# Kernel optimization log

Measured on AMD Instinct MI355X. Metric: run time of the kernel, lower is better.

The kernel has to match this reference:

```python
import jax, jax.numpy as jnp
import numpy as np

B = 16384      # batch
H = 1024       # latent_dim
C = 2          # output_dim (classes)
PPC = 24       # prototypes per class
P = C * PPC    # 48 total prototypes
EPS = 1e-4


def setup_inputs() -> dict:
    key = jax.random.key(0)
    k1, k2, k3, k4, k5 = jax.random.split(key, 5)
    specific_user = jax.random.normal(k1, (B, H), jnp.float32)
    shared_user = jax.random.normal(k2, (B, H), jnp.float32)
    prototype_vectors = jax.random.normal(k3, (P, H), jnp.float32)
    # last_layer weight set by set_last_layer_incorrect_connection(-0.5):
    # +1 for the prototype's own class, -0.5 elsewhere; shape [C, P]
    cls = np.arange(P) // PPC
    ident = (cls[None, :] == np.arange(C)[:, None]).astype(np.float32)
    last_layer_w = jnp.asarray(ident * 1.0 + (1.0 - ident) * (-0.5))
    # nn.Bilinear(H, H, 1): weight [1, H, H], bias [1]
    bilinear_w = jax.random.normal(k4, (1, H, H), jnp.float32) / np.sqrt(H)
    bilinear_b = jax.random.normal(k5, (1,), jnp.float32) * 0.01
    return {
        "specific_user": specific_user,
        "shared_user": shared_user,
        "prototype_vectors": prototype_vectors,
        "last_layer_w": last_layer_w,
        "bilinear_w": bilinear_w,
        "bilinear_b": bilinear_b,
        "flag": 1,
    }


def reference(specific_user, shared_user, prototype_vectors, last_layer_w,
              bilinear_w, bilinear_b, flag):
    # prototype_distances: squared euclid via mm + norms, then log-similarity
    x2 = jnp.sum(specific_user ** 2, axis=1, keepdims=True)          # [B,1]
    p2 = jnp.sum(prototype_vectors ** 2, axis=1)                     # [P]
    distance = -2.0 * (specific_user @ prototype_vectors.T) + x2 + p2[None, :]  # [B,P]
    similarity = jnp.log((distance + 1.0) / (distance + EPS))        # [B,P]
    logits = similarity @ last_layer_w.T                             # [B,C]

    # select the class's 24 prototypes (flag picks class 1 or 0; static int)
    idx = 1 if flag else 0
    sub = prototype_vectors.reshape(C, PPC, H)[idx]                  # [PPC,H]

    # prototype_subgraph_distances: per original broadcast, each row of
    # all_sim is the batch-mean of the log-similarity -> constant over batch.
    s2 = jnp.sum(sub ** 2, axis=1)                                   # [PPC]
    d = -2.0 * (specific_user @ sub.T) + x2 + s2[None, :]            # [B,PPC]
    sim = jnp.mean(jnp.log((d + 1.0) / (d + EPS)), axis=0)           # [PPC]
    jstar = jnp.argmax(sim)                                          # scalar
    chosen_proto = jnp.broadcast_to(sub[jstar], specific_user.shape) # [B,H]

    # nn.Bilinear(chosen_proto, shared_user) -> [B,1]
    pos = jnp.einsum('bi,ij,bj->b', chosen_proto, bilinear_w[0], shared_user)[:, None] + bilinear_b
    return (pos, shared_user, logits, distance)
```

## Files before the change

### kernel.cpp

```cpp
#include <hip/hip_runtime.h>
#include <hip/hip_bf16.h>

#define BATCH 16384
#define HD    1024
#define NP    48
#define PPC   24
#define EPSV  1e-4f

typedef __attribute__((ext_vector_type(8))) short  short8;
typedef __attribute__((ext_vector_type(4))) float  floatx4;

__device__ __forceinline__ float b2f(unsigned short s) {
    union { unsigned u; float f; } c; c.u = ((unsigned)s) << 16; return c.f;
}
__device__ __forceinline__ unsigned short f2bu(float f) {
    __hip_bfloat16 h = __float2bfloat16(f);
    union { __hip_bfloat16 h; unsigned short u; } c; c.h = h; return c.u;
}

__global__ __launch_bounds__(256) void k_prep(const float* __restrict__ proto,
                                              const float* __restrict__ w2,
                                              const int*   __restrict__ flag,
                                              unsigned short* __restrict__ phi,
                                              unsigned short* __restrict__ plo,
                                              float* __restrict__ p2,
                                              float* __restrict__ gcol,
                                              float* __restrict__ V) {
    const int bid = blockIdx.x;
    const int tid = threadIdx.x;

    if (bid < 48) {
        const int p = bid;
        if (p == 4 && tid < NP) gcol[tid] = 0.f;
        const float* row = proto + (size_t)p * HD;
        float acc = 0.f;
#pragma unroll
        for (int c = 0; c < 4; ++c) {
            const int k = c * 256 + tid;
            const float f = row[k];
            acc += f * f;
            const unsigned short h = f2bu(f);
            phi[(size_t)p * HD + k] = h;
            plo[(size_t)p * HD + k] = f2bu(f - b2f(h));
        }
#pragma unroll
        for (int m = 32; m >= 1; m >>= 1) acc += __shfl_xor(acc, m, 64);
        __shared__ float wsum[4];
        if ((tid & 63) == 0) wsum[tid >> 6] = acc;
        __syncthreads();
        if (tid == 0) p2[p] = wsum[0] + wsum[1] + wsum[2] + wsum[3];
    } else {
        const int q   = bid - 48;
        const int jg  = q >> 4;
        const int cc  = q & 15;
        const int c   = cc * 64 + (tid & 63);
        const int j   = jg * 4 + (tid >> 6);
        const int idx = (flag[0] != 0) ? 1 : 0;
        const float* prow = proto + (size_t)(idx * PPC + j) * HD;
        float acc = 0.f;
#pragma unroll 2
        for (int i = 0; i < HD; i += 4) {
            const floatx4 pv = *(const floatx4*)(prow + i);
            acc += pv[0] * w2[(size_t)(i + 0) * HD + c];
            acc += pv[1] * w2[(size_t)(i + 1) * HD + c];
            acc += pv[2] * w2[(size_t)(i + 2) * HD + c];
            acc += pv[3] * w2[(size_t)(i + 3) * HD + c];
        }
        V[(size_t)j * HD + c] = acc;
    }
}

__global__ __launch_bounds__(256, 4) void k_main(
    const float* __restrict__ x,
    const unsigned short* __restrict__ phi,
    const unsigned short* __restrict__ plo,
    const float* __restrict__ llw,
    const float* __restrict__ p2,
    float* __restrict__ gcol,
    float* __restrict__ out_logits,
    float* __restrict__ out_dist)
{
    __shared__ float lacc[4][64][13];
    __shared__ float lx2[4][16];
    const int wave = threadIdx.x >> 6;
    const int lane = threadIdx.x & 63;
    const int quad = lane >> 4;
    const int lr   = lane & 15;
    const int rb   = blockIdx.x * 16;
    const int ko   = wave * 256;

    const float* xr = x + (size_t)(rb + lr) * HD + ko + quad * 8;
    const unsigned short* ph0 = phi + (size_t)lr * HD + ko + quad * 8;
    const unsigned short* ph1 = ph0 + 16 * HD;
    const unsigned short* ph2 = ph0 + 32 * HD;
    const unsigned short* pl0 = plo + (size_t)lr * HD + ko + quad * 8;
    const unsigned short* pl1 = pl0 + 16 * HD;
    const unsigned short* pl2 = pl0 + 32 * HD;

    floatx4 acc0 = {0.f, 0.f, 0.f, 0.f};
    floatx4 acc1 = {0.f, 0.f, 0.f, 0.f};
    floatx4 acc2 = {0.f, 0.f, 0.f, 0.f};
    float x2p = 0.f;

#pragma unroll 2
    for (int kk = 0; kk < 8; ++kk) {
        const floatx4 xa = *(const floatx4*)(xr + kk * 32);
        const floatx4 xb = *(const floatx4*)(xr + kk * 32 + 4);
        short8 ah, al;
#pragma unroll
        for (int j = 0; j < 4; ++j) {
            const float f = xa[j];
            x2p += f * f;
            const unsigned short h = f2bu(f);
            ah[j] = (short)h;
            al[j] = (short)f2bu(f - b2f(h));
        }
#pragma unroll
        for (int j = 0; j < 4; ++j) {
            const float f = xb[j];
            x2p += f * f;
            const unsigned short h = f2bu(f);
            ah[4 + j] = (short)h;
            al[4 + j] = (short)f2bu(f - b2f(h));
        }
        const short8 bh0 = *(const short8*)(ph0 + kk * 32);
        const short8 bh1 = *(const short8*)(ph1 + kk * 32);
        const short8 bh2 = *(const short8*)(ph2 + kk * 32);
        const short8 bl0 = *(const short8*)(pl0 + kk * 32);
        const short8 bl1 = *(const short8*)(pl1 + kk * 32);
        const short8 bl2 = *(const short8*)(pl2 + kk * 32);
        acc0 = __builtin_amdgcn_mfma_f32_16x16x32_bf16(ah, bh0, acc0, 0, 0, 0);
        acc0 = __builtin_amdgcn_mfma_f32_16x16x32_bf16(ah, bl0, acc0, 0, 0, 0);
        acc0 = __builtin_amdgcn_mfma_f32_16x16x32_bf16(al, bh0, acc0, 0, 0, 0);
        acc1 = __builtin_amdgcn_mfma_f32_16x16x32_bf16(ah, bh1, acc1, 0, 0, 0);
        acc1 = __builtin_amdgcn_mfma_f32_16x16x32_bf16(ah, bl1, acc1, 0, 0, 0);
        acc1 = __builtin_amdgcn_mfma_f32_16x16x32_bf16(al, bh1, acc1, 0, 0, 0);
        acc2 = __builtin_amdgcn_mfma_f32_16x16x32_bf16(ah, bh2, acc2, 0, 0, 0);
        acc2 = __builtin_amdgcn_mfma_f32_16x16x32_bf16(ah, bl2, acc2, 0, 0, 0);
        acc2 = __builtin_amdgcn_mfma_f32_16x16x32_bf16(al, bh2, acc2, 0, 0, 0);
    }
    x2p += __shfl_xor(x2p, 16, 64);
    x2p += __shfl_xor(x2p, 32, 64);

#pragma unroll
    for (int r = 0; r < 4; ++r) {
        lacc[wave][lane][r]     = acc0[r];
        lacc[wave][lane][4 + r] = acc1[r];
        lacc[wave][lane][8 + r] = acc2[r];
    }
    if (quad == 0) lx2[wave][lr] = x2p;
    __syncthreads();
    if (wave != 0) return;

    float facc[12];
#pragma unroll
    for (int i = 0; i < 12; ++i)
        facc[i] = lacc[0][lane][i] + lacc[1][lane][i] + lacc[2][lane][i] + lacc[3][lane][i];
    const float x2full = lx2[0][lr] + lx2[1][lr] + lx2[2][lr] + lx2[3][lr];

    float s0[4] = {0.f, 0.f, 0.f, 0.f};
    float s1[4] = {0.f, 0.f, 0.f, 0.f};

#pragma unroll
    for (int t = 0; t < 3; ++t) {
        const int p = t * 16 + lr;
        const float p2p = p2[p];
        const float w0 = llw[p];
        const float w1 = llw[NP + p];
        float cst = 0.f;
#pragma unroll
        for (int r = 0; r < 4; ++r) {
            const int row = quad * 4 + r;
            const float x2r = __shfl(x2full, row, 64);
            const float d = -2.f * facc[t * 4 + r] + x2r + p2p;
            out_dist[(size_t)(rb + row) * NP + p] = d;
            const float sim = log1pf((1.f - EPSV) / (d + EPSV));
            s0[r] += sim * w0;
            s1[r] += sim * w1;
            cst += sim;
        }
        cst += __shfl_xor(cst, 16, 64);
        cst += __shfl_xor(cst, 32, 64);
        if (quad == 0) atomicAdd(&gcol[p], cst);
    }

#pragma unroll
    for (int r = 0; r < 4; ++r) {
        float r0 = s0[r], r1 = s1[r];
#pragma unroll
        for (int m = 1; m <= 8; m <<= 1) {
            r0 += __shfl_xor(r0, m, 64);
            r1 += __shfl_xor(r1, m, 64);
        }
        if (lr == 0) {
            const int brow = rb + quad * 4 + r;
            out_logits[(size_t)brow * 2 + 0] = r0;
            out_logits[(size_t)brow * 2 + 1] = r1;
        }
    }
}

__global__ __launch_bounds__(256) void k_pos(
    const float* __restrict__ sh,
    const float* __restrict__ V,
    const float* __restrict__ gcol,
    const int*   __restrict__ flag,
    const float* __restrict__ bias,
    float* __restrict__ out_pos,
    float* __restrict__ out_copy)
{
    __shared__ int js;
    const int tid  = threadIdx.x;
    if (tid == 0) {
        const int idx = (flag[0] != 0) ? 1 : 0;
        const float* cs = gcol + idx * PPC;
        int bj = 0; float bv = cs[0];
        for (int j = 1; j < PPC; ++j)
            if (cs[j] > bv) { bv = cs[j]; bj = j; }
        js = bj;
    }
    __syncthreads();

    const int wave = tid >> 6;
    const int lane = tid & 63;
    const int b = blockIdx.x * 4 + wave;

    const floatx4* src = (const floatx4*)(sh + (size_t)b * HD);
    floatx4* dst = (floatx4*)(out_copy + (size_t)b * HD);
    const floatx4* vv = (const floatx4*)(V + (size_t)js * HD);
    float acc = 0.f;
#pragma unroll
    for (int c = 0; c < 4; ++c) {
        const int idx2 = c * 64 + lane;
        const floatx4 r = src[idx2];
        __builtin_nontemporal_store(r, &dst[idx2]);
        const floatx4 vr = vv[idx2];
#pragma unroll
        for (int j = 0; j < 4; ++j) acc += r[j] * vr[j];
    }
#pragma unroll
    for (int m = 1; m <= 32; m <<= 1) acc += __shfl_xor(acc, m, 64);
    if (lane == 0) out_pos[b] = acc + bias[0];
}

extern "C" void kernel_launch(void* const* d_in, const int* in_sizes, int n_in,
                              void* d_out, int out_size, void* d_ws, size_t ws_size,
                              hipStream_t stream) {
    const float* x     = (const float*)d_in[0];
    const float* sh    = (const float*)d_in[1];
    const float* proto = (const float*)d_in[2];
    const float* llw   = (const float*)d_in[3];
    const float* w2    = (const float*)d_in[4];
    const float* bb    = (const float*)d_in[5];
    const int*   flag  = (const int*)d_in[6];

    float* out = (float*)d_out;
    float* out_pos    = out;
    float* out_copy   = out + BATCH;
    float* out_logits = out + BATCH + BATCH * HD;
    float* out_dist   = out + BATCH + BATCH * HD + BATCH * 2;

    float* ws_col = (float*)d_ws;
    float* ws_p2  = ws_col + 64;
    float* ws_V   = ws_col + 1024;
    unsigned short* ws_phi = (unsigned short*)(ws_col + 25600);
    unsigned short* ws_plo = ws_phi + NP * HD;

    k_prep<<<144, 256, 0, stream>>>(proto, w2, flag, ws_phi, ws_plo, ws_p2, ws_col, ws_V);
    k_main<<<1024, 256, 0, stream>>>(x, ws_phi, ws_plo, llw, ws_p2, ws_col, out_logits, out_dist);
    k_pos<<<4096, 256, 0, stream>>>(sh, ws_V, ws_col, flag, bb, out_pos, out_copy);
}
```

Measured before the change: 282.6 us.

## Split V=P·W2 over K chunks with register-blocked partials, reduce in main kernel

The prototype-by-bilinear-weight product in the prep kernel is restructured. Before, each thread computed one output column for one prototype over the full 1024-long reduction, rereading W2 once per prototype group. Now each block takes a 64-row slice of W2 and caches the 24 prototype slices in shared memory. Each thread keeps 24 accumulators, so every W2 element is loaded once, and the block writes partial sums to a workspace. Extra blocks appended to the main kernel add up the 16 partials. This costs more workspace traffic and register pressure, and it relies on launch order within the stream so that the reduction runs before k_pos reads V.

```diff
diff --git a/kernel.cpp b/kernel.cpp
--- a/kernel.cpp
+++ b/kernel.cpp
@@ -25,7 +25,7 @@
                                               unsigned short* __restrict__ plo,
                                               float* __restrict__ p2,
                                               float* __restrict__ gcol,
-                                              float* __restrict__ V) {
+                                              float* __restrict__ Vp) {
     const int bid = blockIdx.x;
     const int tid = threadIdx.x;
 
@@ -50,23 +50,32 @@
         __syncthreads();
         if (tid == 0) p2[p] = wsum[0] + wsum[1] + wsum[2] + wsum[3];
     } else {
-        const int q   = bid - 48;
-        const int jg  = q >> 4;
-        const int cc  = q & 15;
-        const int c   = cc * 64 + (tid & 63);
-        const int j   = jg * 4 + (tid >> 6);
+        __shared__ float pl[24][64];
+        const int q  = bid - 48;
+        const int ic = q >> 2;
+        const int cc = q & 3;
+        const int i0 = ic * 64;
+        const int c  = cc * 256 + tid;
         const int idx = (flag[0] != 0) ? 1 : 0;
-        const float* prow = proto + (size_t)(idx * PPC + j) * HD;
-        float acc = 0.f;
-#pragma unroll 2
-        for (int i = 0; i < HD; i += 4) {
-            const floatx4 pv = *(const floatx4*)(prow + i);
-            acc += pv[0] * w2[(size_t)(i + 0) * HD + c];
-            acc += pv[1] * w2[(size_t)(i + 1) * HD + c];
-            acc += pv[2] * w2[(size_t)(i + 2) * HD + c];
-            acc += pv[3] * w2[(size_t)(i + 3) * HD + c];
-        }
-        V[(size_t)j * HD + c] = acc;
+
+        for (int t = tid; t < 24 * 64; t += 256) {
+            const int j = t >> 6, i = t & 63;
+            pl[j][i] = proto[(size_t)(idx * PPC + j) * HD + i0 + i];
+        }
+        __syncthreads();
+
+        float acc[24];
+#pragma unroll
+        for (int j = 0; j < 24; ++j) acc[j] = 0.f;
+#pragma unroll 4
+        for (int i = 0; i < 64; ++i) {
+            const float w = w2[(size_t)(i0 + i) * HD + c];
+#pragma unroll
+            for (int j = 0; j < 24; ++j) acc[j] += pl[j][i] * w;
+        }
+#pragma unroll
+        for (int j = 0; j < 24; ++j)
+            Vp[((size_t)ic * 24 + j) * HD + c] = acc[j];
     }
 }
 
@@ -76,10 +85,25 @@
     const unsigned short* __restrict__ plo,
     const float* __restrict__ llw,
     const float* __restrict__ p2,
+    const float* __restrict__ Vp,
+    float* __restrict__ V,
     float* __restrict__ gcol,
     float* __restrict__ out_logits,
     float* __restrict__ out_dist)
 {
+    if (blockIdx.x >= 1024) {
+        const int j  = blockIdx.x - 1024;
+        const int c4 = threadIdx.x * 4;
+        floatx4 s = {0.f, 0.f, 0.f, 0.f};
+#pragma unroll
+        for (int ic = 0; ic < 16; ++ic) {
+            const floatx4 v = *(const floatx4*)(Vp + ((size_t)ic * 24 + j) * HD + c4);
+            s[0] += v[0]; s[1] += v[1]; s[2] += v[2]; s[3] += v[3];
+        }
+        *(floatx4*)(V + (size_t)j * HD + c4) = s;
+        return;
+    }
+
     __shared__ float lacc[4][64][13];
     __shared__ float lx2[4][16];
     const int wave = threadIdx.x >> 6;
@@ -265,8 +289,9 @@
     float* ws_V   = ws_col + 1024;
     unsigned short* ws_phi = (unsigned short*)(ws_col + 25600);
     unsigned short* ws_plo = ws_phi + NP * HD;
-
-    k_prep<<<144, 256, 0, stream>>>(proto, w2, flag, ws_phi, ws_plo, ws_p2, ws_col, ws_V);
-    k_main<<<1024, 256, 0, stream>>>(x, ws_phi, ws_plo, llw, ws_p2, ws_col, out_logits, out_dist);
+    float* ws_Vp  = ws_col + 74752;
+
+    k_prep<<<112, 256, 0, stream>>>(proto, w2, flag, ws_phi, ws_plo, ws_p2, ws_col, ws_Vp);
+    k_main<<<1048, 256, 0, stream>>>(x, ws_phi, ws_plo, llw, ws_p2, ws_Vp, ws_V, ws_col, out_logits, out_dist);
     k_pos<<<4096, 256, 0, stream>>>(sh, ws_V, ws_col, flag, bb, out_pos, out_copy);
 }
```

Result: faster. 233.7 us (-17.3%).
